# Performance work log

Hardware: AMD Instinct MI355X
Metric: run time of the kernel (lower is better)

## Reference

```python
import jax, jax.numpy as jnp
import numpy as np

B, N, C_FEAT = 2, 1024, 64
S, K, K_FP = 512, 32, 3
D_MODEL, N_HEAD = 128, 4
EPS_BN = 1e-5


def square_distance(src, dst):
    # src [B,N,3], dst [B,M,3] -> [B,N,M], same expansion as torch version
    d = -2.0 * jnp.einsum('bnc,bmc->bnm', src, dst)
    d = d + jnp.sum(src ** 2, -1)[:, :, None]
    d = d + jnp.sum(dst ** 2, -1)[:, None, :]
    return d


def gather_points(points, idx):
    # points [B,N,C], idx [B,...] int -> [B,...,C]  (index_points)
    return jax.vmap(lambda p, i: p[i])(points, idx)


def fps(xyz, n_samples):
    # furthest point sampling, deterministic start at index 0
    Bs, Np, _ = xyz.shape
    def step(carry, _):
        dist, far = carry
        centroid = jax.vmap(lambda p, i: p[i])(xyz, far)  # [B,3]
        d = jnp.sum((xyz - centroid[:, None, :]) ** 2, -1)
        dist = jnp.minimum(dist, d)
        new_far = jnp.argmax(dist, -1).astype(jnp.int32)
        return (dist, new_far), far
    init = (jnp.full((Bs, Np), 1e10, xyz.dtype), jnp.zeros((Bs,), jnp.int32))
    _, idxs = jax.lax.scan(step, init, None, length=n_samples)
    return idxs.T  # [B,S]


def knn(nsample, xyz, new_xyz):
    d = square_distance(new_xyz, xyz)
    _, idx = jax.lax.top_k(-d, nsample)
    return idx  # [B, n_query, nsample]


def setup_inputs() -> dict:
    key = jax.random.key(0)
    ks = jax.random.split(key, 12)
    Din = 2 * C_FEAT + 3  # 131 = 3 + 2*channels (PreExtraction in_channels)
    def lin(k, fan_in, shape):
        return (jax.random.normal(k, shape, jnp.float32) / np.sqrt(fan_in)).astype(jnp.float32)
    z = lambda n: jnp.zeros((n,), jnp.float32)
    return {
        'xyz': jax.random.normal(ks[0], (B, N, 3), jnp.float32),
        'feats': jax.random.normal(ks[1], (B, N, C_FEAT), jnp.float32),
        'affine_alpha': jnp.ones((1, 1, 1, C_FEAT + 3), jnp.float32),
        'affine_beta': jnp.zeros((1, 1, 1, C_FEAT + 3), jnp.float32),
        'W_t': lin(ks[2], Din, (Din, D_MODEL)), 'b_t': z(D_MODEL),
        'bn_g': jnp.ones((D_MODEL,), jnp.float32), 'bn_b': z(D_MODEL),
        'Wq': lin(ks[3], D_MODEL, (D_MODEL, D_MODEL)), 'bq': z(D_MODEL),
        'Wk': lin(ks[4], D_MODEL, (D_MODEL, D_MODEL)), 'bk': z(D_MODEL),
        'Wv': lin(ks[5], D_MODEL, (D_MODEL, D_MODEL)), 'bv': z(D_MODEL),
        'Wo': lin(ks[6], D_MODEL, (D_MODEL, D_MODEL)), 'bo': z(D_MODEL),
        'Wp1': lin(ks[7], 3, (3, D_MODEL)), 'bp1': z(D_MODEL),
        'Wp2': lin(ks[8], D_MODEL, (D_MODEL, N_HEAD)), 'bp2': z(N_HEAD),
    }


def reference(xyz, feats, affine_alpha, affine_beta, W_t, b_t, bn_g, bn_b,
              Wq, bq, Wk, bk, Wv, bv, Wo, bo, Wp1, bp1, Wp2, bp2):
    # ---- LocalGrouper (FPS + KNN + gather + center-normalize + affine) ----
    fps_idx = fps(xyz, S)                       # [B,S]
    new_xyz = gather_points(xyz, fps_idx)       # [B,S,3]
    anchor_feats = gather_points(feats, fps_idx)  # [B,S,C]
    idx = knn(K, xyz, new_xyz)                  # [B,S,K]
    grouped_xyz = gather_points(xyz, idx)       # [B,S,K,3]
    grouped_pts = gather_points(feats, idx)     # [B,S,K,C]
    grouped = jnp.concatenate([grouped_pts, grouped_xyz], -1)  # [B,S,K,C+3]
    mean = jnp.mean(grouped, axis=2, keepdims=True)
    std = jnp.std((grouped - mean).reshape(B, -1), axis=-1, ddof=1)[:, None, None, None]
    grouped = (grouped - mean) / (std + 1e-5)
    grouped = affine_alpha * grouped + affine_beta
    anchor_rep = jnp.broadcast_to(anchor_feats[:, :, None, :], (B, S, K, C_FEAT))
    new_points = jnp.concatenate([grouped, anchor_rep], -1)  # [B,S,K,2C+3]
    # ---- PreExtraction transfer (1x1 conv + BN(eval) + ReLU) + max over K ----
    y = jnp.einsum('bskd,do->bsko', new_points, W_t) + b_t
    y = y * (bn_g / jnp.sqrt(1.0 + EPS_BN)) + bn_b  # BN with running stats (0,1)
    y = jax.nn.relu(y)
    v_k = jnp.max(y, axis=2)                    # [B,S,D_MODEL]
    # ---- PointNetFeaturePropagation (KNN-3 inverse-distance interp) ----
    idx_fp = knn(K_FP, new_xyz, xyz)            # [B,N,3]
    sqrd = square_distance(xyz, new_xyz)        # [B,N,S]
    d_near = jnp.clip(jnp.take_along_axis(sqrd, idx_fp, axis=2), 1e-10, None)
    w = 1.0 / d_near
    w = w / jnp.sum(w, -1, keepdims=True)
    grouped_v = gather_points(v_k, idx_fp)      # [B,N,3,D]
    v_q = jnp.einsum('bnk,bnkc->bnc', w, grouped_v)  # [B,N,D]
    # ---- PointTransformerCrossAttention ----
    Dh = D_MODEL // N_HEAD
    qh = (v_q @ Wq + bq).reshape(B, N, N_HEAD, Dh)
    kh = (v_k @ Wk + bk).reshape(B, S, N_HEAD, Dh)
    vh = (v_k @ Wv + bv).reshape(B, S, N_HEAD, Dh)
    rel = xyz[:, :, None, :] - new_xyz[:, None, :, :]         # [B,N,S,3]
    rpe = jax.nn.relu(rel @ Wp1 + bp1) @ Wp2 + bp2            # [B,N,S,H]
    energy = jnp.einsum('bihd,bjhd->bhij', qh, kh) / jnp.sqrt(jnp.float32(Dh))
    attn = jax.nn.softmax(energy + rpe.transpose(0, 3, 1, 2), axis=-1)
    out = jnp.einsum('bhij,bjhd->bihd', attn, vh).reshape(B, N, D_MODEL)
    return out @ Wo + bo
```

## Files before the change

### kernel.cpp

```cpp
#include <hip/hip_runtime.h>
#include <math.h>

namespace {

constexpr int B  = 2;
constexpr int N  = 1024;
constexpr int CF = 64;
constexpr int S  = 512;
constexpr int K  = 32;
constexpr int DM = 128;
constexpr int NH = 4;
constexpr int DH = 32;
constexpr int GC = 67;
constexpr int DIN = 131;
constexpr int DPAD = 132;
constexpr int EPAD = 516;
constexpr int QB = 4;

typedef float f2 __attribute__((ext_vector_type(2)));

__device__ inline float max3f(float a, float b, float c) { return fmaxf(fmaxf(a, b), c); }
__device__ inline unsigned min3u(unsigned a, unsigned b, unsigned c) { return min(min(a, b), c); }

template <int CTRL>
__device__ inline float dpp_mov_f(float v) {
  return __int_as_float(__builtin_amdgcn_update_dpp(0, __float_as_int(v), CTRL, 0xF, 0xF, true));
}
template <int CTRL>
__device__ inline unsigned dpp_mov_self_u(unsigned v) {
  return (unsigned)__builtin_amdgcn_update_dpp((int)v, (int)v, CTRL, 0xF, 0xF, false);
}

__global__ void __launch_bounds__(64, 1)
fps_kernel(const float* __restrict__ xyz, int* __restrict__ fps_idx,
           float* __restrict__ new_xyz) {
  const int b = blockIdx.x;
  const int lane = threadIdx.x;
  __shared__ __align__(16) float4 pts4[N];
  __shared__ int farhist[S];
  for (int p = lane; p < N; p += 64) {
    pts4[p] = make_float4(xyz[b*N*3 + p*3+0], xyz[b*N*3 + p*3+1], xyz[b*N*3 + p*3+2], 0.0f);
  }
  __syncthreads();
  f2 X[8], Y[8], Z[8];
  float dist[16];
  #pragma unroll
  for (int j = 0; j < 8; ++j) {
    const float4 a = pts4[(2*j)*64 + lane];
    const float4 c = pts4[(2*j+1)*64 + lane];
    X[j] = f2{a.x, c.x}; Y[j] = f2{a.y, c.y}; Z[j] = f2{a.z, c.z};
  }
  #pragma unroll
  for (int k = 0; k < 16; ++k) dist[k] = 1e10f;
  int far = 0;
  for (int s = 0; s < S; ++s) {
    if (lane == 0) farhist[s] = far;
    const float4 c = pts4[far];
    const f2 cx = f2{c.x, c.x}, cy = f2{c.y, c.y}, cz = f2{c.z, c.z};
    #pragma unroll
    for (int j = 0; j < 8; ++j) {
      const f2 dx = X[j] - cx, dy = Y[j] - cy, dz = Z[j] - cz;
      const f2 q = dx*dx + dy*dy + dz*dz;
      dist[2*j]   = fminf(dist[2*j],   q.x);
      dist[2*j+1] = fminf(dist[2*j+1], q.y);
    }
    const float l0 = max3f(dist[0],  dist[1],  dist[2]);
    const float l1 = max3f(dist[3],  dist[4],  dist[5]);
    const float l2 = max3f(dist[6],  dist[7],  dist[8]);
    const float l3 = max3f(dist[9],  dist[10], dist[11]);
    const float l4 = max3f(dist[12], dist[13], dist[14]);
    float mv = fmaxf(max3f(l0, l1, l2), max3f(l3, l4, dist[15]));
    mv = fmaxf(mv, dpp_mov_f<0x111>(mv));
    mv = fmaxf(mv, dpp_mov_f<0x112>(mv));
    mv = fmaxf(mv, dpp_mov_f<0x114>(mv));
    mv = fmaxf(mv, dpp_mov_f<0x118>(mv));
    mv = fmaxf(mv, dpp_mov_f<0x142>(mv));
    mv = fmaxf(mv, dpp_mov_f<0x143>(mv));
    const float maxv = __int_as_float(__builtin_amdgcn_readlane(__float_as_int(mv), 63));
    unsigned cnd[16];
    #pragma unroll
    for (int k = 0; k < 16; ++k) {
      cnd[k] = (dist[k] == maxv) ? (unsigned)(k*64 + lane) : 0xFFFFFFFFu;
    }
    const unsigned u0 = min3u(cnd[0],  cnd[1],  cnd[2]);
    const unsigned u1 = min3u(cnd[3],  cnd[4],  cnd[5]);
    const unsigned u2 = min3u(cnd[6],  cnd[7],  cnd[8]);
    const unsigned u3 = min3u(cnd[9],  cnd[10], cnd[11]);
    const unsigned u4 = min3u(cnd[12], cnd[13], cnd[14]);
    unsigned cand = min(min3u(u0, u1, u2), min3u(u3, u4, cnd[15]));
    cand = min(cand, dpp_mov_self_u<0x111>(cand));
    cand = min(cand, dpp_mov_self_u<0x112>(cand));
    cand = min(cand, dpp_mov_self_u<0x114>(cand));
    cand = min(cand, dpp_mov_self_u<0x118>(cand));
    cand = min(cand, dpp_mov_self_u<0x142>(cand));
    cand = min(cand, dpp_mov_self_u<0x143>(cand));
    far = __builtin_amdgcn_readlane((int)cand, 63);
  }
  __syncthreads();
  for (int s = lane; s < S; s += 64) {
    const int f = farhist[s];
    const float4 c = pts4[f];
    fps_idx[b*S+s] = f;
    new_xyz[(b*S+s)*3+0] = c.x;
    new_xyz[(b*S+s)*3+1] = c.y;
    new_xyz[(b*S+s)*3+2] = c.z;
  }
}

__global__ void knn_kernel(const float* __restrict__ xyz, const float* __restrict__ feats,
                           const float* __restrict__ new_xyz, int* __restrict__ knn_idx,
                           float* __restrict__ mean_out, float2* __restrict__ partials) {
  const int b = blockIdx.y;
  const int tid = threadIdx.x;
  const int wave = tid >> 6, lane = tid & 63;
  const int s = blockIdx.x * 4 + wave;
  __shared__ float pts[N*3];
  __shared__ int sidx_s[4][K];
  for (int i = tid; i < N*3; i += 256) pts[i] = xyz[b*N*3 + i];
  __syncthreads();
  const float qx = new_xyz[(b*S+s)*3+0], qy = new_xyz[(b*S+s)*3+1], qz = new_xyz[(b*S+s)*3+2];
  const float qn = qx*qx + qy*qy + qz*qz;
  float d[16];
  #pragma unroll
  for (int j = 0; j < 16; ++j) {
    const int p = j*64 + lane;
    const float px = pts[p*3+0], py = pts[p*3+1], pz = pts[p*3+2];
    const float dot = qx*px + qy*py + qz*pz;
    const float pn  = px*px + py*py + pz*pz;
    d[j] = (-2.0f*dot + qn) + pn;
  }
  unsigned mask = 0xFFFFu;
  for (int k = 0; k < K; ++k) {
    float bv = INFINITY; int bj = 0;
    #pragma unroll
    for (int j = 0; j < 16; ++j) {
      if (((mask >> j) & 1u) && d[j] < bv) { bv = d[j]; bj = j; }
    }
    int bp = bj*64 + lane;
    #pragma unroll
    for (int m = 1; m < 64; m <<= 1) {
      const float ov = __shfl_xor(bv, m);
      const int   op = __shfl_xor(bp, m);
      if (ov < bv || (ov == bv && op < bp)) { bv = ov; bp = op; }
    }
    if (lane == 0) { knn_idx[(b*S+s)*K + k] = bp; sidx_s[wave][k] = bp; }
    if ((bp & 63) == lane) mask &= ~(1u << (bp >> 6));
  }
  const int bs = b*S + s;
  float ls = 0.0f, lsq = 0.0f;
  float v[K];
  {
    const int c = lane;
    float sum = 0.0f;
    #pragma unroll
    for (int k = 0; k < K; ++k) {
      const int p = sidx_s[wave][k];
      const float g = feats[(b*N+p)*CF + c];
      v[k] = g; sum += g;
    }
    const float mean = sum * (1.0f/K);
    mean_out[bs*GC + c] = mean;
    #pragma unroll
    for (int k = 0; k < K; ++k) {
      const float cc = v[k] - mean;
      ls += cc; lsq += cc*cc;
    }
  }
  if (lane < 3) {
    const int c = CF + lane;
    float sum = 0.0f;
    #pragma unroll
    for (int k = 0; k < K; ++k) {
      const int p = sidx_s[wave][k];
      const float g = xyz[(b*N+p)*3 + lane];
      v[k] = g; sum += g;
    }
    const float mean = sum * (1.0f/K);
    mean_out[bs*GC + c] = mean;
    #pragma unroll
    for (int k = 0; k < K; ++k) {
      const float cc = v[k] - mean;
      ls += cc; lsq += cc*cc;
    }
  }
  #pragma unroll
  for (int m = 1; m < 64; m <<= 1) { ls += __shfl_xor(ls, m); lsq += __shfl_xor(lsq, m); }
  if (lane == 0) partials[bs] = make_float2(ls, lsq);
}

__global__ void stats_kernel(const float2* __restrict__ partials, float* __restrict__ invstd) {
  const int b = blockIdx.x;
  const int lane = threadIdx.x;
  double su = 0.0, sq = 0.0;
  for (int i = lane; i < S; i += 64) {
    const float2 p = partials[b*S+i];
    su += (double)p.x; sq += (double)p.y;
  }
  #pragma unroll
  for (int m = 1; m < 64; m <<= 1) { su += __shfl_xor(su, m); sq += __shfl_xor(sq, m); }
  if (lane == 0) {
    const double nn = (double)S * K * GC;
    const double var = (sq - su*su/nn) / (nn - 1.0);
    invstd[b] = 1.0f / ((float)sqrt(var) + 1e-5f);
  }
}

__global__ void transfer_kernel(const float* __restrict__ feats, const float* __restrict__ xyz,
                                const int* __restrict__ knn_idx, const int* __restrict__ fps_idx,
                                const float* __restrict__ mean_in, const float* __restrict__ invstd,
                                const float* __restrict__ alpha, const float* __restrict__ beta,
                                const float* __restrict__ W_t, const float* __restrict__ b_t,
                                const float* __restrict__ bn_g, const float* __restrict__ bn_b,
                                const float* __restrict__ Wk, const float* __restrict__ bk,
                                const float* __restrict__ Wv, const float* __restrict__ bv,
                                float* __restrict__ v_k, float* __restrict__ kpb,
                                float* __restrict__ vpb) {
  const int bs = blockIdx.x;
  const int b = bs / S;
  const int t = threadIdx.x;
  __shared__ __align__(16) float np_s[K][DPAD];
  __shared__ float vrow[DM];
  __shared__ int sidx[K];
  __shared__ int sanchor;
  if (t < K) sidx[t] = knn_idx[bs*K + t];
  if (t == 0) sanchor = fps_idx[bs];
  __syncthreads();
  const float sinv = invstd[b];
  for (int k = 0; k < K; ++k) {
    const int p = sidx[k];
    for (int c = t; c < DPAD; c += 128) {
      float val = 0.0f;
      if (c < GC) {
        const float g = (c < CF) ? feats[(b*N+p)*CF + c] : xyz[(b*N+p)*3 + (c-CF)];
        val = (g - mean_in[bs*GC + c]) * sinv * alpha[c] + beta[c];
      } else if (c < DIN) {
        val = feats[(b*N+sanchor)*CF + (c - GC)];
      }
      np_s[k][c] = val;
    }
  }
  __syncthreads();
  float acc[K];
  const float bt = b_t[t];
  #pragma unroll
  for (int k = 0; k < K; ++k) acc[k] = bt;
  for (int d4 = 0; d4 < DPAD/4; ++d4) {
    const int d = d4*4;
    const float w0 = W_t[(d+0)*DM + t];
    const float w1 = W_t[(d+1)*DM + t];
    const float w2 = W_t[(d+2)*DM + t];
    const float w3 = (d+3 < DIN) ? W_t[(d+3)*DM + t] : 0.0f;
    #pragma unroll
    for (int k = 0; k < K; ++k) {
      const float4 f = *reinterpret_cast<const float4*>(&np_s[k][d]);
      acc[k] = acc[k] + f.x*w0 + f.y*w1 + f.z*w2 + f.w*w3;
    }
  }
  const float scale = bn_g[t] / sqrtf(1.0f + 1e-5f);
  const float shift = bn_b[t];
  float mx = -INFINITY;
  #pragma unroll
  for (int k = 0; k < K; ++k) {
    const float y = fmaxf(acc[k]*scale + shift, 0.0f);
    mx = fmaxf(mx, y);
  }
  v_k[bs*DM + t] = mx;
  vrow[t] = mx;
  __syncthreads();
  float acck = bk[t], accv = bv[t];
  for (int d = 0; d < DM; ++d) {
    const float f = vrow[d];
    acck += f * Wk[d*DM + t];
    accv += f * Wv[d*DM + t];
  }
  kpb[bs*DM + t] = acck;
  vpb[bs*DM + t] = accv;
}

__global__ void interp_kernel(const float* __restrict__ xyz, const float* __restrict__ new_xyz,
                              const float* __restrict__ v_k, const float* __restrict__ Wq,
                              const float* __restrict__ bq, float* __restrict__ qbuf) {
  const int b = blockIdx.y;
  const int tid = threadIdx.x;
  const int wave = tid >> 6, lane = tid & 63;
  const int n = blockIdx.x*4 + wave;
  __shared__ float pts[S*3];
  __shared__ float vqs[4][DM];
  for (int i = tid; i < S*3; i += 256) pts[i] = new_xyz[b*S*3 + i];
  __syncthreads();
  const float qx = xyz[(b*N+n)*3+0], qy = xyz[(b*N+n)*3+1], qz = xyz[(b*N+n)*3+2];
  const float qn = qx*qx + qy*qy + qz*qz;
  float d[8];
  #pragma unroll
  for (int j = 0; j < 8; ++j) {
    const int p = j*64 + lane;
    const float px = pts[p*3+0], py = pts[p*3+1], pz = pts[p*3+2];
    const float dot = qx*px + qy*py + qz*pz;
    const float pn  = px*px + py*py + pz*pz;
    d[j] = (-2.0f*dot + qn) + pn;
  }
  unsigned mask = 0xFFu;
  float sd[3]; int sp[3];
  #pragma unroll
  for (int k = 0; k < 3; ++k) {
    float bv = INFINITY; int bj = 0;
    #pragma unroll
    for (int j = 0; j < 8; ++j) {
      if (((mask >> j) & 1u) && d[j] < bv) { bv = d[j]; bj = j; }
    }
    int bp = bj*64 + lane;
    #pragma unroll
    for (int m = 1; m < 64; m <<= 1) {
      const float ov = __shfl_xor(bv, m);
      const int   op = __shfl_xor(bp, m);
      if (ov < bv || (ov == bv && op < bp)) { bv = ov; bp = op; }
    }
    sd[k] = bv; sp[k] = bp;
    if ((bp & 63) == lane) mask &= ~(1u << (bp >> 6));
  }
  float w0 = 1.0f / fmaxf(sd[0], 1e-10f);
  float w1 = 1.0f / fmaxf(sd[1], 1e-10f);
  float w2 = 1.0f / fmaxf(sd[2], 1e-10f);
  const float wsum = w0 + w1 + w2;
  w0 /= wsum; w1 /= wsum; w2 /= wsum;
  const float* vk0 = v_k + (b*S + sp[0])*DM;
  const float* vk1 = v_k + (b*S + sp[1])*DM;
  const float* vk2 = v_k + (b*S + sp[2])*DM;
  #pragma unroll
  for (int c = lane; c < DM; c += 64) {
    vqs[wave][c] = w0*vk0[c] + w1*vk1[c] + w2*vk2[c];
  }
  __syncthreads();
  const float* row = vqs[wave];
  #pragma unroll
  for (int half = 0; half < 2; ++half) {
    const int c = lane + half*64;
    float acc = bq[c];
    for (int d = 0; d < DM; ++d) acc += row[d] * Wq[d*DM + c];
    qbuf[(b*N+n)*DM + c] = acc;
  }
}

__global__ void attn_kernel(const float* __restrict__ xyz, const float* __restrict__ new_xyz,
                            const float* __restrict__ qb, const float* __restrict__ kp,
                            const float* __restrict__ vp, const float* __restrict__ Wp1,
                            const float* __restrict__ bp1, const float* __restrict__ Wp2,
                            const float* __restrict__ bp2, const float* __restrict__ Wo,
                            const float* __restrict__ bo, float* __restrict__ out) {
  const int bn0 = blockIdx.x * QB;
  const int b = bn0 / N;
  const int t = threadIdx.x;
  __shared__ __align__(16) float e[QB][NH][EPAD];
  __shared__ __align__(16) float qn_s[QB][DM];
  __shared__ float oa[QB][DM];
  __shared__ float ssum[QB][NH];
  qn_s[t >> 7][t & 127] = qb[(bn0 + (t >> 7))*DM + (t & 127)];
  __syncthreads();
  float qxs[QB], qys[QB], qzs[QB];
  #pragma unroll
  for (int qq = 0; qq < QB; ++qq) {
    qxs[qq] = xyz[(bn0+qq)*3+0];
    qys[qq] = xyz[(bn0+qq)*3+1];
    qzs[qq] = xyz[(bn0+qq)*3+2];
  }
  const float rs = 0.17677669529663687f;
  {
    const int j = t;
    const float px = new_xyz[(b*S+j)*3+0], py = new_xyz[(b*S+j)*3+1], pz = new_xyz[(b*S+j)*3+2];
    float rx[QB], ry[QB], rz[QB];
    float r0[QB], r1[QB], r2[QB], r3[QB];
    #pragma unroll
    for (int qq = 0; qq < QB; ++qq) {
      rx[qq] = qxs[qq]-px; ry[qq] = qys[qq]-py; rz[qq] = qzs[qq]-pz;
      r0[qq] = bp2[0]; r1[qq] = bp2[1]; r2[qq] = bp2[2]; r3[qq] = bp2[3];
    }
    for (int m = 0; m < DM; ++m) {
      const float w1 = Wp1[m], w2 = Wp1[DM+m], w3 = Wp1[2*DM+m], bb = bp1[m];
      const float p0 = Wp2[m*NH+0], p1 = Wp2[m*NH+1], p2 = Wp2[m*NH+2], p3 = Wp2[m*NH+3];
      #pragma unroll
      for (int qq = 0; qq < QB; ++qq) {
        float hm = rx[qq]*w1 + ry[qq]*w2 + rz[qq]*w3 + bb;
        hm = fmaxf(hm, 0.0f);
        r0[qq] += hm*p0; r1[qq] += hm*p1; r2[qq] += hm*p2; r3[qq] += hm*p3;
      }
    }
    #pragma unroll
    for (int h = 0; h < NH; ++h) {
      const float4* kr4 = reinterpret_cast<const float4*>(kp + (b*S+j)*DM + h*DH);
      float acc[QB];
      #pragma unroll
      for (int qq = 0; qq < QB; ++qq) acc[qq] = 0.0f;
      #pragma unroll
      for (int dd = 0; dd < 8; ++dd) {
        const float4 kv = kr4[dd];
        #pragma unroll
        for (int qq = 0; qq < QB; ++qq) {
          const float* qr = &qn_s[qq][h*DH + dd*4];
          acc[qq] += qr[0]*kv.x + qr[1]*kv.y + qr[2]*kv.z + qr[3]*kv.w;
        }
      }
      e[0][h][j] = acc[0]*rs + ((h==0)?r0[0]:(h==1)?r1[0]:(h==2)?r2[0]:r3[0]);
      e[1][h][j] = acc[1]*rs + ((h==0)?r0[1]:(h==1)?r1[1]:(h==2)?r2[1]:r3[1]);
      e[2][h][j] = acc[2]*rs + ((h==0)?r0[2]:(h==1)?r1[2]:(h==2)?r2[2]:r3[2]);
      e[3][h][j] = acc[3]*rs + ((h==0)?r0[3]:(h==1)?r1[3]:(h==2)?r2[3]:r3[3]);
    }
  }
  __syncthreads();
  const int qq = t >> 7;
  const int tt = t & 127;
  const int h = tt >> 5, g = tt & 31;
  {
    float mx = -INFINITY;
    for (int j = g; j < S; j += 32) mx = fmaxf(mx, e[qq][h][j]);
    #pragma unroll
    for (int m = 16; m >= 1; m >>= 1) mx = fmaxf(mx, __shfl_xor(mx, m));
    float sum = 0.0f;
    for (int j = g; j < S; j += 32) { const float ex = expf(e[qq][h][j]-mx); e[qq][h][j] = ex; sum += ex; }
    #pragma unroll
    for (int m = 16; m >= 1; m >>= 1) sum += __shfl_xor(sum, m);
    if (g == 0) ssum[qq][h] = sum;
  }
  __syncthreads();
  {
    float acc = 0.0f;
    for (int j = 0; j < S; j += 4) {
      const float4 ev = *reinterpret_cast<const float4*>(&e[qq][h][j]);
      acc += ev.x * vp[(b*S+j+0)*DM + tt];
      acc += ev.y * vp[(b*S+j+1)*DM + tt];
      acc += ev.z * vp[(b*S+j+2)*DM + tt];
      acc += ev.w * vp[(b*S+j+3)*DM + tt];
    }
    oa[qq][tt] = acc / ssum[qq][h];
  }
  __syncthreads();
  {
    float facc = bo[tt];
    for (int d = 0; d < DM; ++d) facc += oa[qq][d] * Wo[d*DM + tt];
    out[(bn0+qq)*DM + tt] = facc;
  }
}

}

extern "C" void kernel_launch(void* const* d_in, const int* in_sizes, int n_in,
                              void* d_out, int out_size, void* d_ws, size_t ws_size,
                              hipStream_t stream) {
  const float* xyz   = (const float*)d_in[0];
  const float* feats = (const float*)d_in[1];
  const float* alpha = (const float*)d_in[2];
  const float* beta  = (const float*)d_in[3];
  const float* W_t   = (const float*)d_in[4];
  const float* b_t   = (const float*)d_in[5];
  const float* bn_g  = (const float*)d_in[6];
  const float* bn_b  = (const float*)d_in[7];
  const float* Wq = (const float*)d_in[8];  const float* bq = (const float*)d_in[9];
  const float* Wk = (const float*)d_in[10]; const float* bk = (const float*)d_in[11];
  const float* Wv = (const float*)d_in[12]; const float* bv = (const float*)d_in[13];
  const float* Wo = (const float*)d_in[14]; const float* bo = (const float*)d_in[15];
  const float* Wp1= (const float*)d_in[16]; const float* bp1= (const float*)d_in[17];
  const float* Wp2= (const float*)d_in[18]; const float* bp2= (const float*)d_in[19];

  char* w = (char*)d_ws;
  int*    fps_i = (int*)   (w + 0);
  float*  nxyz  = (float*) (w + 4096);
  int*    knn_i = (int*)   (w + 16384);
  float*  meanb = (float*) (w + 147456);
  float2* part  = (float2*)(w + 421888);
  float*  invs  = (float*) (w + 430080);
  float*  vk    = (float*) (w + 430336);
  float*  qbuf  = (float*) (w + 2003200);
  float*  kpb   = (float*) (w + 3051776);
  float*  vpb   = (float*) (w + 3576064);
  float*  outf  = (float*)d_out;

  fps_kernel<<<B, 64, 0, stream>>>(xyz, fps_i, nxyz);
  knn_kernel<<<dim3(S/4, B), 256, 0, stream>>>(xyz, feats, nxyz, knn_i, meanb, part);
  stats_kernel<<<B, 64, 0, stream>>>(part, invs);
  transfer_kernel<<<B*S, 128, 0, stream>>>(feats, xyz, knn_i, fps_i, meanb, invs,
                                           alpha, beta, W_t, b_t, bn_g, bn_b,
                                           Wk, bk, Wv, bv, vk, kpb, vpb);
  interp_kernel<<<dim3(N/4, B), 256, 0, stream>>>(xyz, nxyz, vk, Wq, bq, qbuf);
  attn_kernel<<<(B*N)/QB, 512, 0, stream>>>(xyz, nxyz, qbuf, kpb, vpb, Wp1, bp1, Wp2, bp2, Wo, bo, outf);
}
```

Baseline: 381.6 us.

## Double attention block to 1024 threads, splitting RPE MLP, heads and PV over halves

```diff
diff --git a/kernel.cpp b/kernel.cpp
--- a/kernel.cpp
+++ b/kernel.cpp
@@ -352,41 +352,59 @@
   const int t = threadIdx.x;
   __shared__ __align__(16) float e[QB][NH][EPAD];
   __shared__ __align__(16) float qn_s[QB][DM];
-  __shared__ float oa[QB][DM];
+  __shared__ float oa2[2][QB][DM];
   __shared__ float ssum[QB][NH];
-  qn_s[t >> 7][t & 127] = qb[(bn0 + (t >> 7))*DM + (t & 127)];
-  __syncthreads();
-  float qxs[QB], qys[QB], qzs[QB];
-  #pragma unroll
-  for (int qq = 0; qq < QB; ++qq) {
-    qxs[qq] = xyz[(bn0+qq)*3+0];
-    qys[qq] = xyz[(bn0+qq)*3+1];
-    qzs[qq] = xyz[(bn0+qq)*3+2];
-  }
+  float* rpart = &e[0][0][0];
+  if (t < 512) qn_s[t >> 7][t & 127] = qb[(bn0 + (t >> 7))*DM + (t & 127)];
+  __syncthreads();
+  const int col  = t & 511;
+  const int half = t >> 9;
   const float rs = 0.17677669529663687f;
+  float eout[QB][2];
   {
-    const int j = t;
-    const float px = new_xyz[(b*S+j)*3+0], py = new_xyz[(b*S+j)*3+1], pz = new_xyz[(b*S+j)*3+2];
+    const float px = new_xyz[(b*S+col)*3+0], py = new_xyz[(b*S+col)*3+1], pz = new_xyz[(b*S+col)*3+2];
     float rx[QB], ry[QB], rz[QB];
-    float r0[QB], r1[QB], r2[QB], r3[QB];
+    float r[QB][NH];
     #pragma unroll
     for (int qq = 0; qq < QB; ++qq) {
-      rx[qq] = qxs[qq]-px; ry[qq] = qys[qq]-py; rz[qq] = qzs[qq]-pz;
-      r0[qq] = bp2[0]; r1[qq] = bp2[1]; r2[qq] = bp2[2]; r3[qq] = bp2[3];
-    }
-    for (int m = 0; m < DM; ++m) {
+      rx[qq] = xyz[(bn0+qq)*3+0] - px;
+      ry[qq] = xyz[(bn0+qq)*3+1] - py;
+      rz[qq] = xyz[(bn0+qq)*3+2] - pz;
+      #pragma unroll
+      for (int h = 0; h < NH; ++h) r[qq][h] = (half == 0) ? bp2[h] : 0.0f;
+    }
+    const int m0 = half * 64;
+    for (int m = m0; m < m0 + 64; ++m) {
       const float w1 = Wp1[m], w2 = Wp1[DM+m], w3 = Wp1[2*DM+m], bb = bp1[m];
       const float p0 = Wp2[m*NH+0], p1 = Wp2[m*NH+1], p2 = Wp2[m*NH+2], p3 = Wp2[m*NH+3];
       #pragma unroll
       for (int qq = 0; qq < QB; ++qq) {
         float hm = rx[qq]*w1 + ry[qq]*w2 + rz[qq]*w3 + bb;
         hm = fmaxf(hm, 0.0f);
-        r0[qq] += hm*p0; r1[qq] += hm*p1; r2[qq] += hm*p2; r3[qq] += hm*p3;
+        r[qq][0] += hm*p0; r[qq][1] += hm*p1; r[qq][2] += hm*p2; r[qq][3] += hm*p3;
       }
     }
-    #pragma unroll
-    for (int h = 0; h < NH; ++h) {
-      const float4* kr4 = reinterpret_cast<const float4*>(kp + (b*S+j)*DM + h*DH);
+    if (half == 1) {
+      #pragma unroll
+      for (int qq = 0; qq < QB; ++qq)
+        #pragma unroll
+        for (int h = 0; h < NH; ++h) rpart[col*16 + qq*4 + h] = r[qq][h];
+    }
+    __syncthreads();
+    if (half == 0) {
+      #pragma unroll
+      for (int qq = 0; qq < QB; ++qq)
+        #pragma unroll
+        for (int h = 0; h < NH; ++h) {
+          r[qq][h] += rpart[col*16 + qq*4 + h];
+          rpart[col*16 + qq*4 + h] = r[qq][h];
+        }
+    }
+    __syncthreads();
+    #pragma unroll
+    for (int hh = 0; hh < 2; ++hh) {
+      const int h = half*2 + hh;
+      const float4* kr4 = reinterpret_cast<const float4*>(kp + (b*S+col)*DM + h*DH);
       float acc[QB];
       #pragma unroll
       for (int qq = 0; qq < QB; ++qq) acc[qq] = 0.0f;
@@ -399,17 +417,21 @@
           acc[qq] += qr[0]*kv.x + qr[1]*kv.y + qr[2]*kv.z + qr[3]*kv.w;
         }
       }
-      e[0][h][j] = acc[0]*rs + ((h==0)?r0[0]:(h==1)?r1[0]:(h==2)?r2[0]:r3[0]);
-      e[1][h][j] = acc[1]*rs + ((h==0)?r0[1]:(h==1)?r1[1]:(h==2)?r2[1]:r3[1]);
-      e[2][h][j] = acc[2]*rs + ((h==0)?r0[2]:(h==1)?r1[2]:(h==2)?r2[2]:r3[2]);
-      e[3][h][j] = acc[3]*rs + ((h==0)?r0[3]:(h==1)?r1[3]:(h==2)?r2[3]:r3[3]);
-    }
-  }
-  __syncthreads();
-  const int qq = t >> 7;
-  const int tt = t & 127;
-  const int h = tt >> 5, g = tt & 31;
-  {
+      #pragma unroll
+      for (int qq = 0; qq < QB; ++qq) eout[qq][hh] = acc[qq]*rs + rpart[col*16 + qq*4 + h];
+    }
+  }
+  __syncthreads();
+  #pragma unroll
+  for (int hh = 0; hh < 2; ++hh) {
+    const int h = half*2 + hh;
+    #pragma unroll
+    for (int qq = 0; qq < QB; ++qq) e[qq][h][col] = eout[qq][hh];
+  }
+  __syncthreads();
+  if (t < 512) {
+    const int qq = t >> 7, tt = t & 127;
+    const int h = tt >> 5, g = tt & 31;
     float mx = -INFINITY;
     for (int j = g; j < S; j += 32) mx = fmaxf(mx, e[qq][h][j]);
     #pragma unroll
@@ -422,20 +444,32 @@
   }
   __syncthreads();
   {
+    const int grp = t >> 7;
+    const int qq3 = grp >> 1, jh = grp & 1;
+    const int tt = t & 127;
+    const int h3 = tt >> 5;
     float acc = 0.0f;
-    for (int j = 0; j < S; j += 4) {
-      const float4 ev = *reinterpret_cast<const float4*>(&e[qq][h][j]);
+    const int j0 = jh * 256;
+    for (int j = j0; j < j0 + 256; j += 4) {
+      const float4 ev = *reinterpret_cast<const float4*>(&e[qq3][h3][j]);
       acc += ev.x * vp[(b*S+j+0)*DM + tt];
       acc += ev.y * vp[(b*S+j+1)*DM + tt];
       acc += ev.z * vp[(b*S+j+2)*DM + tt];
       acc += ev.w * vp[(b*S+j+3)*DM + tt];
     }
-    oa[qq][tt] = acc / ssum[qq][h];
-  }
-  __syncthreads();
-  {
+    oa2[jh][qq3][tt] = acc;
+  }
+  __syncthreads();
+  if (t < 512) {
+    const int qq = t >> 7, tt = t & 127;
+    const int h = tt >> 5;
+    oa2[0][qq][tt] = (oa2[0][qq][tt] + oa2[1][qq][tt]) / ssum[qq][h];
+  }
+  __syncthreads();
+  if (t < 512) {
+    const int qq = t >> 7, tt = t & 127;
     float facc = bo[tt];
-    for (int d = 0; d < DM; ++d) facc += oa[qq][d] * Wo[d*DM + tt];
+    for (int d = 0; d < DM; ++d) facc += oa2[0][qq][d] * Wo[d*DM + tt];
     out[(bn0+qq)*DM + tt] = facc;
   }
 }
@@ -480,5 +514,5 @@
                                            alpha, beta, W_t, b_t, bn_g, bn_b,
                                            Wk, bk, Wv, bv, vk, kpb, vpb);
   interp_kernel<<<dim3(N/4, B), 256, 0, stream>>>(xyz, nxyz, vk, Wq, bq, qbuf);
-  attn_kernel<<<(B*N)/QB, 512, 0, stream>>>(xyz, nxyz, qbuf, kpb, vpb, Wp1, bp1, Wp2, bp2, Wo, bo, outf);
-}
+  attn_kernel<<<(B*N)/QB, 1024, 0, stream>>>(xyz, nxyz, qbuf, kpb, vpb, Wp1, bp1, Wp2, bp2, Wo, bo, outf);
+}
```

Result: slower. 417.6 us (+9.4%).
